# Kernel optimization log

Hardware: AMD Instinct MI355X
Metric: run time of the kernel (lower is better)

## Reference

```python
import jax, jax.numpy as jnp
import numpy as np

EPS = 1e-18
MARGIN = 0.2  # hp.margin (cancels: positive/positive == 1)
BIAS = 1.0    # hp.bias


def setup_inputs() -> dict:
    key = jax.random.key(0)
    k1, k2, k3, k4 = jax.random.split(key, 4)
    B, T, D = 32, 256, 256  # T == D required by the broadcast in Ecos_sim
    return {
        "pre_VF": jax.random.normal(k1, (B, T, D), dtype=jnp.float32),
        "pre_AF": jax.random.normal(k2, (B, T, D), dtype=jnp.float32),
        "back_VF": jax.random.normal(k3, (B, T, D), dtype=jnp.float32),
        "back_AF": jax.random.normal(k4, (B, T, D), dtype=jnp.float32),
    }


def _direction_loss(V, A):
    """For each anchor i: log(1 + sum_{j != i} exp(sim(V_i, A_j))).

    sim(V_i, A_j)[t, s] = (V_i @ A_j.T)[t, s] / (||V_i||_F * colnorm(A_j)[s])
    (faithful to Ecos_sim: scalar Frobenius norm for V, per-column norm for A,
    broadcast along the last axis; positive/positive == 1 exactly, so the
    positive term and margin cancel.)
    """
    B = V.shape[0]
    # upper[i,j,t,s] = <V[i,t,:], A[j,s,:]>
    upper = jnp.einsum("itd,jsd->ijts", V, A)
    v_norm = jnp.sqrt(jnp.sum(V ** 2, axis=(1, 2)) + EPS)      # [B]
    a_norm = jnp.sqrt(jnp.sum(A ** 2, axis=1) + EPS)           # [B, D]
    sim = upper / (v_norm[:, None, None, None] * a_norm[None, :, None, :])
    e_sim = jnp.exp(sim)                                        # [B,B,T,T]
    idx = jnp.arange(B)
    down = e_sim.sum(axis=1) - e_sim[idx, idx]                  # exclude j == i
    rows = jnp.log(1.0 + down)                                  # [B,T,T]
    return rows.reshape(-1, rows.shape[-1])                     # cat along dim 0


def reference(pre_VF, pre_AF, back_VF, back_AF):
    sim_back_V = _direction_loss(back_VF, back_AF)
    sim_back_A = _direction_loss(back_AF, back_VF)
    return -(1.0 / BIAS) * (sim_back_V + sim_back_A)
```

## Files before the change

kernel.cpp:

```cpp
#include <hip/hip_runtime.h>
#include <cstdint>

#define R_TOT 8192
#define KD    256
#define SLOT  ((size_t)R_TOT * KD)
#define IVN_OFF  0
#define ICN_OFF  256
#define CSQ_OFF  (ICN_OFF + 65536)
#define MATS_OFF (CSQ_OFF + 524288)
#define PART_OFF (MATS_OFF + 2 * SLOT)

typedef float f32x4 __attribute__((ext_vector_type(4)));
typedef short s16x8 __attribute__((ext_vector_type(8)));
typedef long  lx2   __attribute__((ext_vector_type(2)));

__device__ __forceinline__ unsigned short bf16rne(float x){
  union { float f; uint32_t u; } c; c.f = x;
  return (unsigned short)((c.u + 0x7fffu + ((c.u >> 16) & 1u)) >> 16);
}
__device__ __forceinline__ float bf2f(unsigned short u){
  union { uint32_t u; float f; } c; c.u = ((uint32_t)u) << 16; return c.f;
}
__device__ __forceinline__ void glds16(const void* g, void* l){
  __builtin_amdgcn_global_load_lds((const __attribute__((address_space(1))) uint32_t*)g,
                                   (__attribute__((address_space(3))) uint32_t*)l, 16, 0, 0);
}

__global__ void cast_ns_k(const float* __restrict__ V, const float* __restrict__ A,
                          unsigned char* __restrict__ mats, float* __restrict__ csq){
  const int tc = blockIdx.x, j = blockIdx.y, ten = blockIdx.z;
  const int tid = threadIdx.x;
  const int g    = tid & 31;
  const int tsub = tid >> 5;
  const int q    = ((g >> 3) << 2) | (g & 3);
  const int half = (g >> 2) & 1;
  const float* X = (ten ? A : V) + (size_t)j * 65536;
  unsigned char* M = mats + (size_t)ten * SLOT + (size_t)j * 65536;
  float cs[8];
  #pragma unroll
  for (int e = 0; e < 8; ++e) cs[e] = 0.f;
  #pragma unroll
  for (int tt = 0; tt < 4; ++tt){
    const int t = tc * 32 + tt * 8 + tsub;
    const float4 p0 = *(const float4*)(X + t * 256 + g * 8);
    const float4 p1 = *(const float4*)(X + t * 256 + g * 8 + 4);
    cs[0] += p0.x * p0.x; cs[1] += p0.y * p0.y; cs[2] += p0.z * p0.z; cs[3] += p0.w * p0.w;
    cs[4] += p1.x * p1.x; cs[5] += p1.y * p1.y; cs[6] += p1.z * p1.z; cs[7] += p1.w * p1.w;
    int d0 = __builtin_amdgcn_cvt_pk_fp8_f32(p0.x, p0.y, 0, false);
    d0     = __builtin_amdgcn_cvt_pk_fp8_f32(p0.z, p0.w, d0, true);
    int d1 = __builtin_amdgcn_cvt_pk_fp8_f32(p1.x, p1.y, 0, false);
    d1     = __builtin_amdgcn_cvt_pk_fp8_f32(p1.z, p1.w, d1, true);
    int2 o; o.x = d0; o.y = d1;
    *(int2*)(M + (size_t)t * 256 + (((q ^ (t & 15)) << 4) | (half << 3))) = o;
  }
  __shared__ float red[8][256];
  #pragma unroll
  for (int e = 0; e < 8; ++e) red[tsub][g * 8 + e] = cs[e];
  __syncthreads();
  float s = 0.f;
  #pragma unroll
  for (int gg = 0; gg < 8; ++gg) s += red[gg][tid];
  csq[(size_t)((tc * 2 + ten) * 32 + j) * 256 + tid] = s;
}

__global__ void nreduce_k(const float* __restrict__ csq, float* __restrict__ ivn,
                          float* __restrict__ icn){
  const int j = blockIdx.x, ten = blockIdx.y, s = threadIdx.x;
  float c = 0.f;
  #pragma unroll
  for (int tc = 0; tc < 8; ++tc)
    c += csq[(size_t)((tc * 2 + ten) * 32 + j) * 256 + s];
  icn[ten * 8192 + j * 256 + s] = rsqrtf(c + 1e-18f);
  __shared__ float red[256];
  red[s] = c; __syncthreads();
  for (int off = 128; off > 0; off >>= 1){
    if (s < off) red[s] += red[s + off];
    __syncthreads();
  }
  if (s == 0) ivn[ten * 32 + j] = rsqrtf(red[0] + 1e-18f);
}

__global__ __launch_bounds__(256, 4) void gemm_exp_k(const unsigned char* __restrict__ mats,
                                                     const float* __restrict__ ivn,
                                                     const float* __restrict__ icn,
                                                     unsigned short* __restrict__ part){
  __shared__ __align__(16) char smem[16384];
  const int tid  = threadIdx.x;
  const int lane = tid & 63;
  const int w    = tid >> 6;
  const int wm   = w * 32;
  const int lm   = lane & 15;
  const int kh   = lane >> 4;
  const int dir  = blockIdx.x;
  const int s0   = blockIdx.y * 32;
  const int rb   = blockIdx.z;
  const int r0   = rb * 128;
  const int ib   = rb >> 1;

  const unsigned char* rowmat = mats + (size_t)dir * SLOT;
  const unsigned char* colmat = mats + (size_t)(1 - dir) * SLOT;
  const float sivn = ivn[dir * 32 + ib] * 1.44269504088896340736f;
  const float* icnb = icn + (size_t)(1 - dir) * 8192 + s0 + lm;

  lx2 afr[2][4];
  #pragma unroll
  for (int mi = 0; mi < 2; ++mi){
    const unsigned char* rp = rowmat + (size_t)(r0 + wm + mi * 16 + lm) * 256;
    #pragma unroll
    for (int t = 0; t < 4; ++t)
      afr[mi][t] = *(const lx2*)(rp + (((((t << 2) | kh)) ^ lm) << 4));
  }
  #pragma unroll
  for (int mi = 0; mi < 2; ++mi)
    #pragma unroll
    for (int t = 0; t < 4; ++t)
      asm volatile("" : "+v"(afr[mi][t]));

  int a4[4];
  {
    const int base  = lm * 256 + ((kh ^ (lm & 3)) << 4);
    const int base2 = base ^ ((lm >> 2) << 6);
    #pragma unroll
    for (int t = 0; t < 4; ++t) a4[t] = base2 ^ (t << 6);
  }

  f32x4 acc[2][2];
  #pragma unroll
  for (int mi = 0; mi < 2; ++mi)
    #pragma unroll
    for (int ni = 0; ni < 2; ++ni)
      acc[mi][ni] = f32x4{0.f, 0.f, 0.f, 0.f};

  {
    const int j0 = (ib == 0) ? 1 : 0;
    const unsigned char* src = colmat + ((size_t)j0 * 256 + s0) * 256;
    #pragma unroll
    for (int c = 0; c < 2; ++c)
      glds16(src + (size_t)(c * 256 + tid) * 16, smem + (c * 256 + w * 64) * 16);
  }
  __syncthreads();

  for (int jj = 0; jj < 31; ++jj){
    const int j = jj + (jj >= ib ? 1 : 0);
    if (jj < 30){
      const int jn = (jj + 1) + ((jj + 1) >= ib ? 1 : 0);
      const unsigned char* src = colmat + ((size_t)jn * 256 + s0) * 256;
      char* dst = smem + (((jj + 1) & 1) << 13);
      #pragma unroll
      for (int c = 0; c < 2; ++c)
        glds16(src + (size_t)(c * 256 + tid) * 16, dst + (c * 256 + w * 64) * 16);
    }

    const float csc0 = sivn * icnb[j * 256];
    const float csc1 = sivn * icnb[j * 256 + 16];

    const char* rbuf = smem + ((jj & 1) << 13);
    f32x4 S[2][2];
    #pragma unroll
    for (int mi = 0; mi < 2; ++mi)
      #pragma unroll
      for (int ni = 0; ni < 2; ++ni)
        S[mi][ni] = f32x4{0.f, 0.f, 0.f, 0.f};

    #pragma unroll
    for (int t = 0; t < 4; ++t){
      lx2 b0 = *(const lx2*)(rbuf + a4[t]);
      lx2 b1 = *(const lx2*)(rbuf + a4[t] + 4096);
      S[0][0] = __builtin_amdgcn_mfma_f32_16x16x32_fp8_fp8(afr[0][t][0], b0[0], S[0][0], 0, 0, 0);
      S[1][0] = __builtin_amdgcn_mfma_f32_16x16x32_fp8_fp8(afr[1][t][0], b0[0], S[1][0], 0, 0, 0);
      S[0][1] = __builtin_amdgcn_mfma_f32_16x16x32_fp8_fp8(afr[0][t][0], b1[0], S[0][1], 0, 0, 0);
      S[1][1] = __builtin_amdgcn_mfma_f32_16x16x32_fp8_fp8(afr[1][t][0], b1[0], S[1][1], 0, 0, 0);
      S[0][0] = __builtin_amdgcn_mfma_f32_16x16x32_fp8_fp8(afr[0][t][1], b0[1], S[0][0], 0, 0, 0);
      S[1][0] = __builtin_amdgcn_mfma_f32_16x16x32_fp8_fp8(afr[1][t][1], b0[1], S[1][0], 0, 0, 0);
      S[0][1] = __builtin_amdgcn_mfma_f32_16x16x32_fp8_fp8(afr[0][t][1], b1[1], S[0][1], 0, 0, 0);
      S[1][1] = __builtin_amdgcn_mfma_f32_16x16x32_fp8_fp8(afr[1][t][1], b1[1], S[1][1], 0, 0, 0);
    }
    #pragma unroll
    for (int mi = 0; mi < 2; ++mi)
      #pragma unroll
      for (int r = 0; r < 4; ++r){
        acc[mi][0][r] += __builtin_amdgcn_exp2f(S[mi][0][r] * csc0);
        acc[mi][1][r] += __builtin_amdgcn_exp2f(S[mi][1][r] * csc1);
      }

    __syncthreads();
  }

  unsigned short* ebuf = (unsigned short*)smem;
  #pragma unroll
  for (int mi = 0; mi < 2; ++mi)
    #pragma unroll
    for (int ni = 0; ni < 2; ++ni){
      const int n = ni * 16 + lm;
      #pragma unroll
      for (int r = 0; r < 4; ++r){
        const int m = wm + mi * 16 + (kh << 2) + r;
        ebuf[m * 40 + n] = bf16rne(acc[mi][ni][r]);
      }
    }
  __syncthreads();
  unsigned short* P = part + (size_t)dir * SLOT;
  #pragma unroll
  for (int p = 0; p < 2; ++p){
    const int q   = tid + p * 256;
    const int row = q >> 2;
    const int c8  = q & 3;
    s16x8 v = *(const s16x8*)(&ebuf[row * 40 + c8 * 8]);
    *(s16x8*)(&P[(size_t)(r0 + row) * 256 + s0 + c8 * 8]) = v;
  }
}

__global__ void combine_k(const unsigned short* __restrict__ part, float* __restrict__ out){
  const int idx = blockIdx.x * 256 + threadIdx.x;
  s16x8 a = ((const s16x8*)part)[idx];
  s16x8 b = ((const s16x8*)(part + (size_t)R_TOT * 256))[idx];
  float4 o0, o1;
  o0.x = -(__logf(1.f + bf2f((unsigned short)a[0])) + __logf(1.f + bf2f((unsigned short)b[0])));
  o0.y = -(__logf(1.f + bf2f((unsigned short)a[1])) + __logf(1.f + bf2f((unsigned short)b[1])));
  o0.z = -(__logf(1.f + bf2f((unsigned short)a[2])) + __logf(1.f + bf2f((unsigned short)b[2])));
  o0.w = -(__logf(1.f + bf2f((unsigned short)a[3])) + __logf(1.f + bf2f((unsigned short)b[3])));
  o1.x = -(__logf(1.f + bf2f((unsigned short)a[4])) + __logf(1.f + bf2f((unsigned short)b[4])));
  o1.y = -(__logf(1.f + bf2f((unsigned short)a[5])) + __logf(1.f + bf2f((unsigned short)b[5])));
  o1.z = -(__logf(1.f + bf2f((unsigned short)a[6])) + __logf(1.f + bf2f((unsigned short)b[6])));
  o1.w = -(__logf(1.f + bf2f((unsigned short)a[7])) + __logf(1.f + bf2f((unsigned short)b[7])));
  ((float4*)out)[idx * 2]     = o0;
  ((float4*)out)[idx * 2 + 1] = o1;
}

extern "C" void kernel_launch(void* const* d_in, const int* in_sizes, int n_in,
                              void* d_out, int out_size, void* d_ws, size_t ws_size,
                              hipStream_t stream){
  const float* V = (const float*)d_in[2];
  const float* A = (const float*)d_in[3];
  float* out = (float*)d_out;
  float* ivn = (float*)((char*)d_ws + IVN_OFF);
  float* icn = (float*)((char*)d_ws + ICN_OFF);
  float* csq = (float*)((char*)d_ws + CSQ_OFF);
  unsigned char* mats = (unsigned char*)((char*)d_ws + MATS_OFF);
  unsigned short* part = (unsigned short*)((char*)d_ws + PART_OFF);

  cast_ns_k<<<dim3(8, 32, 2), 256, 0, stream>>>(V, A, mats, csq);
  nreduce_k<<<dim3(32, 2), 256, 0, stream>>>(csq, ivn, icn);
  gemm_exp_k<<<dim3(2, 8, 64), 256, 0, stream>>>(mats, ivn, icn, part);
  combine_k<<<1024, 256, 0, stream>>>(part, out);
}
```

Measured before the change: 130.3 us.

## Fuse both directions and log-combine into the GEMM-exp kernel

Each block now handles both similarity directions for a 64x32 output tile, accumulating the exp sums for each direction in registers and writing the final -(log(1+a)+log(1+b)) directly to the output. This removes the bf16 partial buffer, its write and re-read, and the separate combine kernel launch, and drops the bf16 rounding of the partial sums. Each wave's tile shrinks from 32x32 to 32x16, so there are fewer MFMAs per shared-memory load. Each block runs two sequential 31-step loops with the same total grid size (1024 blocks), which may change latency hiding.

New measurement: 133.8 us. +2.7%, slower.

```diff
diff --git a/kernel.cpp b/kernel.cpp
--- a/kernel.cpp
+++ b/kernel.cpp
@@ -8,19 +8,10 @@
 #define ICN_OFF  256
 #define CSQ_OFF  (ICN_OFF + 65536)
 #define MATS_OFF (CSQ_OFF + 524288)
-#define PART_OFF (MATS_OFF + 2 * SLOT)
 
 typedef float f32x4 __attribute__((ext_vector_type(4)));
-typedef short s16x8 __attribute__((ext_vector_type(8)));
 typedef long  lx2   __attribute__((ext_vector_type(2)));
 
-__device__ __forceinline__ unsigned short bf16rne(float x){
-  union { float f; uint32_t u; } c; c.f = x;
-  return (unsigned short)((c.u + 0x7fffu + ((c.u >> 16) & 1u)) >> 16);
-}
-__device__ __forceinline__ float bf2f(unsigned short u){
-  union { uint32_t u; float f; } c; c.u = ((uint32_t)u) << 16; return c.f;
-}
 __device__ __forceinline__ void glds16(const void* g, void* l){
   __builtin_amdgcn_global_load_lds((const __attribute__((address_space(1))) uint32_t*)g,
                                    (__attribute__((address_space(3))) uint32_t*)l, 16, 0, 0);
@@ -80,41 +71,23 @@
   if (s == 0) ivn[ten * 32 + j] = rsqrtf(red[0] + 1e-18f);
 }
 
-__global__ __launch_bounds__(256, 4) void gemm_exp_k(const unsigned char* __restrict__ mats,
-                                                     const float* __restrict__ ivn,
-                                                     const float* __restrict__ icn,
-                                                     unsigned short* __restrict__ part){
+__global__ __launch_bounds__(256, 4) void gemm_both_k(const unsigned char* __restrict__ mats,
+                                                      const float* __restrict__ ivn,
+                                                      const float* __restrict__ icn,
+                                                      float* __restrict__ out){
   __shared__ __align__(16) char smem[16384];
   const int tid  = threadIdx.x;
   const int lane = tid & 63;
   const int w    = tid >> 6;
-  const int wm   = w * 32;
+  const int wm   = (w & 1) * 32;
+  const int wn   = (w >> 1) * 16;
+  const int wno  = wn << 8;
   const int lm   = lane & 15;
   const int kh   = lane >> 4;
-  const int dir  = blockIdx.x;
-  const int s0   = blockIdx.y * 32;
-  const int rb   = blockIdx.z;
-  const int r0   = rb * 128;
-  const int ib   = rb >> 1;
-
-  const unsigned char* rowmat = mats + (size_t)dir * SLOT;
-  const unsigned char* colmat = mats + (size_t)(1 - dir) * SLOT;
-  const float sivn = ivn[dir * 32 + ib] * 1.44269504088896340736f;
-  const float* icnb = icn + (size_t)(1 - dir) * 8192 + s0 + lm;
-
-  lx2 afr[2][4];
-  #pragma unroll
-  for (int mi = 0; mi < 2; ++mi){
-    const unsigned char* rp = rowmat + (size_t)(r0 + wm + mi * 16 + lm) * 256;
-    #pragma unroll
-    for (int t = 0; t < 4; ++t)
-      afr[mi][t] = *(const lx2*)(rp + (((((t << 2) | kh)) ^ lm) << 4));
-  }
-  #pragma unroll
-  for (int mi = 0; mi < 2; ++mi)
-    #pragma unroll
-    for (int t = 0; t < 4; ++t)
-      asm volatile("" : "+v"(afr[mi][t]));
+  const int s0   = blockIdx.x * 32;
+  const int rb   = blockIdx.y;
+  const int r0   = rb * 64;
+  const int ib   = rb >> 2;
 
   int a4[4];
   {
@@ -124,107 +97,98 @@
     for (int t = 0; t < 4; ++t) a4[t] = base2 ^ (t << 6);
   }
 
-  f32x4 acc[2][2];
-  #pragma unroll
-  for (int mi = 0; mi < 2; ++mi)
-    #pragma unroll
-    for (int ni = 0; ni < 2; ++ni)
-      acc[mi][ni] = f32x4{0.f, 0.f, 0.f, 0.f};
-
-  {
-    const int j0 = (ib == 0) ? 1 : 0;
-    const unsigned char* src = colmat + ((size_t)j0 * 256 + s0) * 256;
-    #pragma unroll
-    for (int c = 0; c < 2; ++c)
-      glds16(src + (size_t)(c * 256 + tid) * 16, smem + (c * 256 + w * 64) * 16);
+  f32x4 accd[2][2];
+  #pragma unroll
+  for (int d = 0; d < 2; ++d)
+    #pragma unroll
+    for (int mi = 0; mi < 2; ++mi)
+      accd[d][mi] = f32x4{0.f, 0.f, 0.f, 0.f};
+
+  #pragma unroll
+  for (int dir = 0; dir < 2; ++dir){
+    const unsigned char* rowmat = mats + (size_t)dir * SLOT;
+    const unsigned char* colmat = mats + (size_t)(1 - dir) * SLOT;
+    const float sivn = ivn[dir * 32 + ib] * 1.44269504088896340736f;
+    const float* icnb = icn + (size_t)(1 - dir) * 8192 + s0 + wn + lm;
+
+    lx2 afr[2][4];
+    #pragma unroll
+    for (int mi = 0; mi < 2; ++mi){
+      const unsigned char* rp = rowmat + (size_t)(r0 + wm + mi * 16 + lm) * 256;
+      #pragma unroll
+      for (int t = 0; t < 4; ++t)
+        afr[mi][t] = *(const lx2*)(rp + (((((t << 2) | kh)) ^ lm) << 4));
+    }
+    #pragma unroll
+    for (int mi = 0; mi < 2; ++mi)
+      #pragma unroll
+      for (int t = 0; t < 4; ++t)
+        asm volatile("" : "+v"(afr[mi][t]));
+
+    {
+      const int j0 = (ib == 0) ? 1 : 0;
+      const unsigned char* src = colmat + ((size_t)j0 * 256 + s0) * 256;
+      #pragma unroll
+      for (int c = 0; c < 2; ++c)
+        glds16(src + (size_t)(c * 256 + tid) * 16, smem + (c * 256 + w * 64) * 16);
+    }
+    __syncthreads();
+
+    for (int jj = 0; jj < 31; ++jj){
+      const int j = jj + (jj >= ib ? 1 : 0);
+      if (jj < 30){
+        const int jn = (jj + 1) + ((jj + 1) >= ib ? 1 : 0);
+        const unsigned char* src = colmat + ((size_t)jn * 256 + s0) * 256;
+        char* dst = smem + (((jj + 1) & 1) << 13);
+        #pragma unroll
+        for (int c = 0; c < 2; ++c)
+          glds16(src + (size_t)(c * 256 + tid) * 16, dst + (c * 256 + w * 64) * 16);
+      }
+
+      const float csc = sivn * icnb[j * 256];
+
+      const char* rbuf = smem + ((jj & 1) << 13);
+      f32x4 S[2];
+      S[0] = f32x4{0.f, 0.f, 0.f, 0.f};
+      S[1] = f32x4{0.f, 0.f, 0.f, 0.f};
+
+      #pragma unroll
+      for (int t = 0; t < 4; ++t){
+        lx2 b = *(const lx2*)(rbuf + a4[t] + wno);
+        S[0] = __builtin_amdgcn_mfma_f32_16x16x32_fp8_fp8(afr[0][t][0], b[0], S[0], 0, 0, 0);
+        S[1] = __builtin_amdgcn_mfma_f32_16x16x32_fp8_fp8(afr[1][t][0], b[0], S[1], 0, 0, 0);
+        S[0] = __builtin_amdgcn_mfma_f32_16x16x32_fp8_fp8(afr[0][t][1], b[1], S[0], 0, 0, 0);
+        S[1] = __builtin_amdgcn_mfma_f32_16x16x32_fp8_fp8(afr[1][t][1], b[1], S[1], 0, 0, 0);
+      }
+      #pragma unroll
+      for (int mi = 0; mi < 2; ++mi)
+        #pragma unroll
+        for (int r = 0; r < 4; ++r)
+          accd[dir][mi][r] += __builtin_amdgcn_exp2f(S[mi][r] * csc);
+
+      __syncthreads();
+    }
+  }
+
+  float* ebuf = (float*)smem;
+  #pragma unroll
+  for (int mi = 0; mi < 2; ++mi){
+    const int n = wn + lm;
+    #pragma unroll
+    for (int r = 0; r < 4; ++r){
+      const int m = wm + mi * 16 + (kh << 2) + r;
+      const float p0 = accd[0][mi][r], p1 = accd[1][mi][r];
+      ebuf[m * 36 + n] = -(__logf(1.f + p0) + __logf(1.f + p1));
+    }
   }
   __syncthreads();
-
-  for (int jj = 0; jj < 31; ++jj){
-    const int j = jj + (jj >= ib ? 1 : 0);
-    if (jj < 30){
-      const int jn = (jj + 1) + ((jj + 1) >= ib ? 1 : 0);
-      const unsigned char* src = colmat + ((size_t)jn * 256 + s0) * 256;
-      char* dst = smem + (((jj + 1) & 1) << 13);
-      #pragma unroll
-      for (int c = 0; c < 2; ++c)
-        glds16(src + (size_t)(c * 256 + tid) * 16, dst + (c * 256 + w * 64) * 16);
-    }
-
-    const float csc0 = sivn * icnb[j * 256];
-    const float csc1 = sivn * icnb[j * 256 + 16];
-
-    const char* rbuf = smem + ((jj & 1) << 13);
-    f32x4 S[2][2];
-    #pragma unroll
-    for (int mi = 0; mi < 2; ++mi)
-      #pragma unroll
-      for (int ni = 0; ni < 2; ++ni)
-        S[mi][ni] = f32x4{0.f, 0.f, 0.f, 0.f};
-
-    #pragma unroll
-    for (int t = 0; t < 4; ++t){
-      lx2 b0 = *(const lx2*)(rbuf + a4[t]);
-      lx2 b1 = *(const lx2*)(rbuf + a4[t] + 4096);
-      S[0][0] = __builtin_amdgcn_mfma_f32_16x16x32_fp8_fp8(afr[0][t][0], b0[0], S[0][0], 0, 0, 0);
-      S[1][0] = __builtin_amdgcn_mfma_f32_16x16x32_fp8_fp8(afr[1][t][0], b0[0], S[1][0], 0, 0, 0);
-      S[0][1] = __builtin_amdgcn_mfma_f32_16x16x32_fp8_fp8(afr[0][t][0], b1[0], S[0][1], 0, 0, 0);
-      S[1][1] = __builtin_amdgcn_mfma_f32_16x16x32_fp8_fp8(afr[1][t][0], b1[0], S[1][1], 0, 0, 0);
-      S[0][0] = __builtin_amdgcn_mfma_f32_16x16x32_fp8_fp8(afr[0][t][1], b0[1], S[0][0], 0, 0, 0);
-      S[1][0] = __builtin_amdgcn_mfma_f32_16x16x32_fp8_fp8(afr[1][t][1], b0[1], S[1][0], 0, 0, 0);
-      S[0][1] = __builtin_amdgcn_mfma_f32_16x16x32_fp8_fp8(afr[0][t][1], b1[1], S[0][1], 0, 0, 0);
-      S[1][1] = __builtin_amdgcn_mfma_f32_16x16x32_fp8_fp8(afr[1][t][1], b1[1], S[1][1], 0, 0, 0);
-    }
-    #pragma unroll
-    for (int mi = 0; mi < 2; ++mi)
-      #pragma unroll
-      for (int r = 0; r < 4; ++r){
-        acc[mi][0][r] += __builtin_amdgcn_exp2f(S[mi][0][r] * csc0);
-        acc[mi][1][r] += __builtin_amdgcn_exp2f(S[mi][1][r] * csc1);
-      }
-
-    __syncthreads();
-  }
-
-  unsigned short* ebuf = (unsigned short*)smem;
-  #pragma unroll
-  for (int mi = 0; mi < 2; ++mi)
-    #pragma unroll
-    for (int ni = 0; ni < 2; ++ni){
-      const int n = ni * 16 + lm;
-      #pragma unroll
-      for (int r = 0; r < 4; ++r){
-        const int m = wm + mi * 16 + (kh << 2) + r;
-        ebuf[m * 40 + n] = bf16rne(acc[mi][ni][r]);
-      }
-    }
-  __syncthreads();
-  unsigned short* P = part + (size_t)dir * SLOT;
   #pragma unroll
   for (int p = 0; p < 2; ++p){
-    const int q   = tid + p * 256;
-    const int row = q >> 2;
-    const int c8  = q & 3;
-    s16x8 v = *(const s16x8*)(&ebuf[row * 40 + c8 * 8]);
-    *(s16x8*)(&P[(size_t)(r0 + row) * 256 + s0 + c8 * 8]) = v;
-  }
-}
-
-__global__ void combine_k(const unsigned short* __restrict__ part, float* __restrict__ out){
-  const int idx = blockIdx.x * 256 + threadIdx.x;
-  s16x8 a = ((const s16x8*)part)[idx];
-  s16x8 b = ((const s16x8*)(part + (size_t)R_TOT * 256))[idx];
-  float4 o0, o1;
-  o0.x = -(__logf(1.f + bf2f((unsigned short)a[0])) + __logf(1.f + bf2f((unsigned short)b[0])));
-  o0.y = -(__logf(1.f + bf2f((unsigned short)a[1])) + __logf(1.f + bf2f((unsigned short)b[1])));
-  o0.z = -(__logf(1.f + bf2f((unsigned short)a[2])) + __logf(1.f + bf2f((unsigned short)b[2])));
-  o0.w = -(__logf(1.f + bf2f((unsigned short)a[3])) + __logf(1.f + bf2f((unsigned short)b[3])));
-  o1.x = -(__logf(1.f + bf2f((unsigned short)a[4])) + __logf(1.f + bf2f((unsigned short)b[4])));
-  o1.y = -(__logf(1.f + bf2f((unsigned short)a[5])) + __logf(1.f + bf2f((unsigned short)b[5])));
-  o1.z = -(__logf(1.f + bf2f((unsigned short)a[6])) + __logf(1.f + bf2f((unsigned short)b[6])));
-  o1.w = -(__logf(1.f + bf2f((unsigned short)a[7])) + __logf(1.f + bf2f((unsigned short)b[7])));
-  ((float4*)out)[idx * 2]     = o0;
-  ((float4*)out)[idx * 2 + 1] = o1;
+    const int i   = tid + p * 256;
+    const int row = i >> 3;
+    const int c4  = i & 7;
+    *(f32x4*)(&out[(size_t)(r0 + row) * 256 + s0 + c4 * 4]) = *(const f32x4*)(&ebuf[row * 36 + c4 * 4]);
+  }
 }
 
 extern "C" void kernel_launch(void* const* d_in, const int* in_sizes, int n_in,
@@ -237,10 +201,8 @@
   float* icn = (float*)((char*)d_ws + ICN_OFF);
   float* csq = (float*)((char*)d_ws + CSQ_OFF);
   unsigned char* mats = (unsigned char*)((char*)d_ws + MATS_OFF);
-  unsigned short* part = (unsigned short*)((char*)d_ws + PART_OFF);
 
   cast_ns_k<<<dim3(8, 32, 2), 256, 0, stream>>>(V, A, mats, csq);
   nreduce_k<<<dim3(32, 2), 256, 0, stream>>>(csq, ivn, icn);
-  gemm_exp_k<<<dim3(2, 8, 64), 256, 0, stream>>>(mats, ivn, icn, part);
-  combine_k<<<1024, 256, 0, stream>>>(part, out);
-}
+  gemm_both_k<<<dim3(8, 128), 256, 0, stream>>>(mats, ivn, icn, out);
+}
```
